# Performance work log

Hardware: AMD Instinct MI355X
Metric: run time of the kernel (lower is better)

## Reference

```python
import jax, jax.numpy as jnp
from jax import lax
import numpy as np

NUM_HEAD = 12
EPS = 1e-5            # torch LayerNorm default
NEG_INF = 1.0e12      # self.inf_value in the source
LEAKY_SLOPE = 0.01    # torch LeakyReLU default
MASK_FIRST = True     # maskedAtten=True applies only to block 0


def _layer_norm(x, s, b):
    m = jnp.mean(x, axis=-1, keepdims=True)
    v = jnp.var(x, axis=-1, keepdims=True)
    return (x - m) / jnp.sqrt(v + EPS) * s + b


def _forward(x, conv_w, conv_b, pos, ln0_s, ln0_b, Wq, bq, Wk, bk, Wv, bv,
             Wo, bo, ln1_s, ln1_b, W1, b1, W2, b2, proj_w, proj_b):
    B, C, H, W = x.shape
    E = conv_w.shape[0]
    P = conv_w.shape[-1]
    hd = E // NUM_HEAD

    # patch embed: Conv2d(C, E, P, stride=P)
    h = lax.conv_general_dilated(x, conv_w, (P, P), 'VALID',
                                 dimension_numbers=('NCHW', 'OIHW', 'NCHW'))
    h = h + conv_b[None, :, None, None]
    L = h.shape[2] * h.shape[3]
    h = h.reshape(B, E, L).transpose(0, 2, 1) + pos  # (B, L, E)

    causal = jnp.triu(jnp.ones((L, L), dtype=bool), 1)
    n_layers = Wq.shape[0]
    for i in range(n_layers):
        # --- attention block ---
        xn = _layer_norm(h, ln0_s[i], ln0_b[i])
        q = (xn @ Wq[i] + bq[i]).reshape(B, L, NUM_HEAD, hd).transpose(0, 2, 1, 3)
        k = (xn @ Wk[i] + bk[i]).reshape(B, L, NUM_HEAD, hd).transpose(0, 2, 1, 3)
        v = (xn @ Wv[i] + bv[i]).reshape(B, L, NUM_HEAD, hd).transpose(0, 2, 1, 3)
        scores = jnp.einsum('bhqd,bhkd->bhqk', q, k) * (hd ** -0.5)
        if i == 0 and MASK_FIRST:
            scores = jnp.where(causal, -NEG_INF, scores)
        a = jax.nn.softmax(scores, axis=-1)
        o = jnp.einsum('bhqk,bhkd->bhqd', a, v)  # (B, NH, L, hd)
        # faithful to torch source: reshape(bs, l, emb) WITHOUT permuting heads back
        o = o.reshape(B, L, E)
        o = o @ Wo[i] + bo[i]
        h = o + h  # residual onto pre-LN input
        # --- MLP block ---
        xr = _layer_norm(h, ln1_s[i], ln1_b[i])
        m = xr @ W1[i] + b1[i]
        m = jnp.where(m >= 0, m, LEAKY_SLOPE * m)
        m = m @ W2[i] + b2[i]
        h = m + xr  # residual onto post-LN (as in source)

    y = h @ proj_w + proj_b               # (B, L, C*P*P)
    y = y.transpose(0, 2, 1).reshape(B, C, H, W)
    return y


def setup_inputs() -> dict:
    key = jax.random.key(0)
    B, C, H, W = 8, 3, 384, 384
    P, E, NL = 16, 768, 8
    FF = 4 * E
    L = (H // P) * (W // P)  # 576
    CPP = C * P * P          # 768
    s = 0.02
    ks = jax.random.split(key, 24)
    f32 = jnp.float32
    inp = {
        'x': jax.random.normal(ks[0], (B, C, H, W), f32),
        'conv_w': jax.random.normal(ks[1], (E, C, P, P), f32) * s,
        'conv_b': jax.random.normal(ks[2], (E,), f32) * s,
        'pos': jax.random.normal(ks[3], (1, L, E), f32),
        'ln0_s': jnp.ones((NL, E), f32),
        'ln0_b': jnp.zeros((NL, E), f32),
        'Wq': jax.random.normal(ks[4], (NL, E, E), f32) * s,
        'bq': jax.random.normal(ks[5], (NL, E), f32) * s,
        'Wk': jax.random.normal(ks[6], (NL, E, E), f32) * s,
        'bk': jax.random.normal(ks[7], (NL, E), f32) * s,
        'Wv': jax.random.normal(ks[8], (NL, E, E), f32) * s,
        'bv': jax.random.normal(ks[9], (NL, E), f32) * s,
        'Wo': jax.random.normal(ks[10], (NL, E, E), f32) * s,
        'bo': jax.random.normal(ks[11], (NL, E), f32) * s,
        'ln1_s': jnp.ones((NL, E), f32),
        'ln1_b': jnp.zeros((NL, E), f32),
        'W1': jax.random.normal(ks[12], (NL, E, FF), f32) * s,
        'b1': jax.random.normal(ks[13], (NL, FF), f32) * s,
        'W2': jax.random.normal(ks[14], (NL, FF, E), f32) * s,
        'b2': jax.random.normal(ks[15], (NL, E), f32) * s,
        'proj_w': jax.random.normal(ks[16], (E, CPP), f32) * s,
        'proj_b': jax.random.normal(ks[17], (CPP,), f32) * s,
    }
    return inp


def reference(x, conv_w, conv_b, pos, ln0_s, ln0_b, Wq, bq, Wk, bk, Wv, bv,
              Wo, bo, ln1_s, ln1_b, W1, b1, W2, b2, proj_w, proj_b):
    return _forward(x, conv_w, conv_b, pos, ln0_s, ln0_b, Wq, bq, Wk, bk,
                    Wv, bv, Wo, bo, ln1_s, ln1_b, W1, b1, W2, b2,
                    proj_w, proj_b)
```

## Files before the change

### kernel.cpp

```cpp
#include <hip/hip_runtime.h>
#include <hip/hip_bf16.h>
#include <stdint.h>

#define NLAYERS 8
#define LSEQ 576
#define EMB 768
#define NHEAD 12
#define HDIM 64
#define FFDIM 3072
#define BLROWS 4608

typedef __attribute__((ext_vector_type(8))) short short8;
typedef __attribute__((ext_vector_type(4))) short short4v;
typedef __attribute__((ext_vector_type(4))) float floatx4;

__device__ __forceinline__ float b2f(short s) {
    union { float f; uint32_t u; } x; x.u = ((uint32_t)(uint16_t)s) << 16; return x.f;
}
__device__ __forceinline__ short f2b(float f) {
    union { float f; uint32_t u; } x; x.f = f;
    uint32_t r = x.u + 0x7fffu + ((x.u >> 16) & 1u);
    return (short)(r >> 16);
}

#define GLDS16(gp, lp) __builtin_amdgcn_global_load_lds( \
    (const __attribute__((address_space(1))) void*)(gp), \
    (__attribute__((address_space(3))) void*)(lp), 16, 0, 0)

__device__ __forceinline__ void xcd_remap(int& bx, int& by) {
    const int gx = gridDim.x;
    const int n  = gx * gridDim.y;
    const int orig = by * gx + bx;
    const int q = n >> 3, r = n & 7;
    const int xcd = orig & 7;
    const int wgid = (xcd < r ? xcd * (q + 1) : r * (q + 1) + (xcd - r) * q) + (orig >> 3);
    bx = wgid % gx;
    by = wgid / gx;
}

template<int DEPTH, int RES, bool ADD_POS, bool LEAKY, int OUTM, bool QKV, bool SPLITK>
__global__ __launch_bounds__(256)
void gemm_bt(const short* __restrict__ A, const short* __restrict__ Bt,
             const float* __restrict__ bias, const float* __restrict__ pos,
             const void* __restrict__ res, void* __restrict__ Cout,
             short* __restrict__ aux_kp, short* __restrict__ aux_vt,
             int N, int K)
{
    __shared__ short As[DEPTH * 64 * 64];
    __shared__ short Bs[DEPTH * 128 * 64];
    int bx = blockIdx.x, by = blockIdx.y;
    xcd_remap(bx, by);
    const int t    = threadIdx.x;
    const int lane = t & 63;
    const int w    = t >> 6;
    const int m0   = by * 64;
    const int n0   = bx * 128;
    const int wm   = (w >> 1) * 32;
    const int wn   = (w & 1) * 64;

    const int klen  = SPLITK ? (K >> 1) : K;
    const int kbase = SPLITK ? blockIdx.z * klen : 0;

    floatx4 acc[2][4];
#pragma unroll
    for (int i = 0; i < 2; ++i)
#pragma unroll
        for (int j = 0; j < 4; ++j)
            acc[i][j] = (floatx4){0.f, 0.f, 0.f, 0.f};

    const int srow = t >> 3;
    const int sch  = t & 7;
    const short* Ag = A  + (size_t)m0 * K + kbase;
    const short* Bg = Bt + (size_t)n0 * K + kbase;
    const int nt = klen >> 6;

#define STAGE(buf, k0)                                                              \
    {                                                                               \
        _Pragma("unroll")                                                           \
        for (int i = 0; i < 2; ++i) {                                               \
            int row = srow + i * 32;                                                \
            GLDS16(Ag + (size_t)row * K + (k0) + ((sch ^ (row & 7)) << 3),          \
                   &As[(buf) * 4096 + (size_t)(t + i * 256) * 8]);                  \
        }                                                                           \
        _Pragma("unroll")                                                           \
        for (int i = 0; i < 4; ++i) {                                               \
            int row = srow + i * 32;                                                \
            GLDS16(Bg + (size_t)row * K + (k0) + ((sch ^ (row & 7)) << 3),          \
                   &Bs[(buf) * 8192 + (size_t)(t + i * 256) * 8]);                  \
        }                                                                           \
    }

#define COMPUTE(buf)                                                                \
    {                                                                               \
        _Pragma("unroll")                                                           \
        for (int ks = 0; ks < 2; ++ks) {                                            \
            short8 af[2], bf[4];                                                    \
            _Pragma("unroll")                                                       \
            for (int i = 0; i < 2; ++i) {                                           \
                int row = wm + i * 16 + (lane & 15);                                \
                int ch  = (ks * 4 + (lane >> 4)) ^ (row & 7);                       \
                af[i] = *(const short8*)&As[(buf) * 4096 + row * 64 + ch * 8];      \
            }                                                                       \
            _Pragma("unroll")                                                       \
            for (int j = 0; j < 4; ++j) {                                           \
                int row = wn + j * 16 + (lane & 15);                                \
                int ch  = (ks * 4 + (lane >> 4)) ^ (row & 7);                       \
                bf[j] = *(const short8*)&Bs[(buf) * 8192 + row * 64 + ch * 8];      \
            }                                                                       \
            _Pragma("unroll")                                                       \
            for (int i = 0; i < 2; ++i)                                             \
                _Pragma("unroll")                                                   \
                for (int j = 0; j < 4; ++j)                                         \
                    acc[i][j] = __builtin_amdgcn_mfma_f32_16x16x32_bf16(            \
                        af[i], bf[j], acc[i][j], 0, 0, 0);                          \
        }                                                                           \
    }

    if constexpr (DEPTH == 2) {
        STAGE(0, 0);
        __syncthreads();
        int cur = 0;
        for (int k0 = 0; k0 < klen; k0 += 64) {
            if (k0 + 64 < klen) STAGE(cur ^ 1, k0 + 64);
            COMPUTE(cur);
            __syncthreads();
            cur ^= 1;
        }
    } else {
        STAGE(0, 0);
        STAGE(1, 64);
        asm volatile("s_waitcnt vmcnt(6)" ::: "memory");
        __builtin_amdgcn_sched_barrier(0);
        __builtin_amdgcn_s_barrier();
        int cur = 0, stg = 2;
        for (int tt = 0; tt < nt; ++tt) {
            if (tt + 2 < nt) STAGE(stg, (tt + 2) << 6);
            COMPUTE(cur);
            if (tt + 1 < nt) {
                if (tt + 2 < nt) { asm volatile("s_waitcnt vmcnt(6)" ::: "memory"); }
                else             { asm volatile("s_waitcnt vmcnt(0)" ::: "memory"); }
                __builtin_amdgcn_sched_barrier(0);
                __builtin_amdgcn_s_barrier();
                __builtin_amdgcn_sched_barrier(0);
            }
            cur = (cur + 1 == DEPTH) ? 0 : cur + 1;
            stg = (stg + 1 == DEPTH) ? 0 : stg + 1;
        }
    }
#undef STAGE
#undef COMPUTE

    const int colb = n0 + wn + (lane & 15);
    const int rowb = m0 + wm + ((lane >> 4) * 4);

    if constexpr (SPLITK) {
        float* P = blockIdx.z ? (float*)aux_kp : (float*)Cout;
#pragma unroll
        for (int i = 0; i < 2; ++i)
#pragma unroll
            for (int j = 0; j < 4; ++j)
#pragma unroll
                for (int r = 0; r < 4; ++r)
                    P[(size_t)(rowb + i * 16 + r) * N + colb + j * 16] = acc[i][j][r];
        return;
    }

#pragma unroll
    for (int i = 0; i < 2; ++i) {
#pragma unroll
        for (int j = 0; j < 4; ++j) {
            const int col = colb + j * 16;
            const float bv = bias[col];
#pragma unroll
            for (int r = 0; r < 4; ++r) {
                const int row = rowb + i * 16 + r;
                float v = acc[i][j][r] + bv;
                if constexpr (ADD_POS) v += pos[(size_t)(row % LSEQ) * N + col];
                if constexpr (RES == 1) v += ((const float*)res)[(size_t)row * N + col];
                if constexpr (RES == 2) v += b2f(((const short*)res)[(size_t)row * N + col]);
                if constexpr (LEAKY)   v = v >= 0.f ? v : 0.01f * v;
                if constexpr (QKV) {
                    const int b = row / LSEQ, l = row % LSEQ;
                    const short sv16 = f2b(v);
                    if (col < 768) {
                        ((short*)Cout)[(size_t)row * 768 + col] = sv16;
                    } else if (col < 1536) {
                        const int d = col - 768, hh = d >> 6, dd = d & 63;
                        const size_t bh = (size_t)b * 12 + hh;
                        aux_kp[(bh * LSEQ + l) * 64 + (dd & 7) + (((dd >> 3) ^ (l & 7)) << 3)] = sv16;
                    } else {
                        const int d = col - 1536, hh = d >> 6, dd = d & 63;
                        const size_t bh = (size_t)b * 12 + hh;
                        aux_vt[(bh * 64 + dd) * LSEQ + (l & ~63) + ((l & 63) ^ ((dd & 7) << 3))] = sv16;
                    }
                } else if constexpr (OUTM == 1) {
                    ((float*)Cout)[(size_t)row * N + col] = v;
                } else if constexpr (OUTM == 2) {
                    ((float*)Cout)[(size_t)row * N + col] = v;
                    aux_kp[(size_t)row * N + col] = f2b(v);
                } else {
                    ((short*)Cout)[(size_t)row * N + col] = f2b(v);
                }
            }
        }
    }
}

template<int RES, bool ADD_POS, int OUTM>
__global__ __launch_bounds__(256)
void combinek(const float* __restrict__ P0, const float* __restrict__ P1,
              const float* __restrict__ bias, const float* __restrict__ pos,
              const void* __restrict__ res, float* __restrict__ out,
              short* __restrict__ auxb)
{
    const size_t i4 = ((size_t)blockIdx.x * 256 + threadIdx.x) * 4;
    const int row = (int)(i4 / 768);
    const int col = (int)(i4 % 768);
    floatx4 a = *(const floatx4*)&P0[i4];
    floatx4 b = *(const floatx4*)&P1[i4];
    floatx4 bv = *(const floatx4*)&bias[col];
    floatx4 v;
#pragma unroll
    for (int j = 0; j < 4; ++j) v[j] = a[j] + b[j] + bv[j];
    if constexpr (ADD_POS) {
        floatx4 p = *(const floatx4*)&pos[(size_t)(row % LSEQ) * 768 + col];
#pragma unroll
        for (int j = 0; j < 4; ++j) v[j] += p[j];
    }
    if constexpr (RES == 1) {
        floatx4 rr = *(const floatx4*)&((const float*)res)[i4];
#pragma unroll
        for (int j = 0; j < 4; ++j) v[j] += rr[j];
    }
    if constexpr (RES == 2) {
        short4v rr = *(const short4v*)&((const short*)res)[i4];
#pragma unroll
        for (int j = 0; j < 4; ++j) v[j] += b2f(rr[j]);
    }
    *(floatx4*)&out[i4] = v;
    if constexpr (OUTM == 2) {
        short4v ob;
#pragma unroll
        for (int j = 0; j < 4; ++j) ob[j] = f2b(v[j]);
        *(short4v*)&auxb[i4] = ob;
    }
}

__global__ __launch_bounds__(256)
void ln_kernel(const float* __restrict__ h, const float* __restrict__ g,
               const float* __restrict__ bbias, short* __restrict__ outb)
{
    const int row = blockIdx.x;
    const float* x = h + (size_t)row * EMB;
    const int t = threadIdx.x;
    float v0 = x[t], v1 = x[t + 256], v2 = x[t + 512];
    float s  = v0 + v1 + v2;
    float ss = v0 * v0 + v1 * v1 + v2 * v2;
#pragma unroll
    for (int m = 1; m < 64; m <<= 1) {
        s  += __shfl_xor(s, m, 64);
        ss += __shfl_xor(ss, m, 64);
    }
    __shared__ float red[8];
    if ((t & 63) == 0) { red[t >> 6] = s; red[4 + (t >> 6)] = ss; }
    __syncthreads();
    float S  = red[0] + red[1] + red[2] + red[3];
    float SS = red[4] + red[5] + red[6] + red[7];
    float mean = S * (1.f / 768.f);
    float var  = SS * (1.f / 768.f) - mean * mean;
    float rstd = rsqrtf(var + 1e-5f);
    const size_t base = (size_t)row * EMB;
#pragma unroll
    for (int q = 0; q < 3; ++q) {
        int e = t + q * 256;
        float v = (q == 0 ? v0 : (q == 1 ? v1 : v2));
        float y = (v - mean) * rstd * g[e] + bbias[e];
        outb[base + e] = f2b(y);
    }
}

__global__ __launch_bounds__(256)
void attn_mfma(const short* __restrict__ qbuf, const short* __restrict__ kp,
               const short* __restrict__ vt, short* __restrict__ oout, int causal)
{
    const int qt = blockIdx.x, bh = blockIdx.y;
    const int b = bh / 12, h = bh % 12;
    const int t = threadIdx.x, lane = t & 63, w = t >> 6;

    __shared__ short Ks[64 * 64];
    __shared__ short Vs[64 * 64];
    __shared__ short Plds[4][16][72];

    const int nrow = lane & 15;
    const int kch  = (lane >> 4) * 8;
    const int swz  = (lane & 7) << 3;

    short8 aq[2];
    {
        const short* qrow = qbuf + ((size_t)(b * LSEQ) + qt * 64 + w * 16 + nrow) * 768 + h * 64 + kch;
        aq[0] = *(const short8*)qrow;
        aq[1] = *(const short8*)(qrow + 32);
    }

    float m[4], lsum[4];
    floatx4 oacc[4];
#pragma unroll
    for (int r = 0; r < 4; ++r) { m[r] = -3e38f; lsum[r] = 0.f; }
#pragma unroll
    for (int j = 0; j < 4; ++j) oacc[j] = (floatx4){0.f, 0.f, 0.f, 0.f};

    const int ktend = causal ? qt : 8;
    const short* ksrc = kp + ((size_t)bh * LSEQ) * 64;
    const short* vsrc = vt + ((size_t)bh * 64) * LSEQ;

    for (int kt = 0; kt <= ktend; ++kt) {
        __syncthreads();
        {
            const short* kt_src = ksrc + (size_t)(kt * 64) * 64;
            GLDS16(kt_src + (size_t)t * 8,          &Ks[(size_t)t * 8]);
            GLDS16(kt_src + (size_t)(t + 256) * 8,  &Ks[(size_t)(t + 256) * 8]);
            int f0 = t, f1 = t + 256;
            GLDS16(vsrc + (size_t)(f0 >> 3) * LSEQ + kt * 64 + (f0 & 7) * 8, &Vs[(size_t)f0 * 8]);
            GLDS16(vsrc + (size_t)(f1 >> 3) * LSEQ + kt * 64 + (f1 & 7) * 8, &Vs[(size_t)f1 * 8]);
        }
        __syncthreads();

        floatx4 sc[4];
#pragma unroll
        for (int j = 0; j < 4; ++j) sc[j] = (floatx4){0.f, 0.f, 0.f, 0.f};
#pragma unroll
        for (int s = 0; s < 2; ++s) {
#pragma unroll
            for (int j = 0; j < 4; ++j) {
                short8 bk = *(const short8*)&Ks[(16 * j + nrow) * 64 + ((kch + 32 * s) ^ swz)];
                sc[j] = __builtin_amdgcn_mfma_f32_16x16x32_bf16(aq[s], bk, sc[j], 0, 0, 0);
            }
        }
        float sv[4][4];
#pragma unroll
        for (int j = 0; j < 4; ++j)
#pragma unroll
            for (int r = 0; r < 4; ++r) {
                float v = sc[j][r] * 0.125f;
                if (causal && kt == qt) {
                    int key = kt * 64 + 16 * j + nrow;
                    int qr  = qt * 64 + w * 16 + (lane >> 4) * 4 + r;
                    if (key > qr) v = -1e12f;
                }
                sv[j][r] = v;
            }
#pragma unroll
        for (int r = 0; r < 4; ++r) {
            float tm = fmaxf(fmaxf(sv[0][r], sv[1][r]), fmaxf(sv[2][r], sv[3][r]));
            tm = fmaxf(tm, __shfl_xor(tm, 1, 64));
            tm = fmaxf(tm, __shfl_xor(tm, 2, 64));
            tm = fmaxf(tm, __shfl_xor(tm, 4, 64));
            tm = fmaxf(tm, __shfl_xor(tm, 8, 64));
            float nm = fmaxf(m[r], tm);
            float c  = __expf(m[r] - nm);
            m[r] = nm;
            float ps = 0.f;
#pragma unroll
            for (int j = 0; j < 4; ++j) {
                float p = __expf(sv[j][r] - nm);
                sv[j][r] = p;
                ps += p;
            }
            lsum[r] = lsum[r] * c + ps;
#pragma unroll
            for (int j = 0; j < 4; ++j) oacc[j][r] *= c;
        }
#pragma unroll
        for (int j = 0; j < 4; ++j)
#pragma unroll
            for (int r = 0; r < 4; ++r)
                Plds[w][(lane >> 4) * 4 + r][16 * j + nrow] = f2b(sv[j][r]);
        short8 ap[2];
#pragma unroll
        for (int s = 0; s < 2; ++s)
            ap[s] = *(const short8*)&Plds[w][nrow][kch + 32 * s];
#pragma unroll
        for (int s = 0; s < 2; ++s) {
#pragma unroll
            for (int j = 0; j < 4; ++j) {
                short8 bv = *(const short8*)&Vs[(16 * j + nrow) * 64 + ((kch + 32 * s) ^ swz)];
                oacc[j] = __builtin_amdgcn_mfma_f32_16x16x32_bf16(ap[s], bv, oacc[j], 0, 0, 0);
            }
        }
    }

    float inv[4];
#pragma unroll
    for (int r = 0; r < 4; ++r) {
        float L = lsum[r];
        L += __shfl_xor(L, 1, 64);
        L += __shfl_xor(L, 2, 64);
        L += __shfl_xor(L, 4, 64);
        L += __shfl_xor(L, 8, 64);
        inv[r] = 1.f / L;
    }
#pragma unroll
    for (int j = 0; j < 4; ++j)
#pragma unroll
        for (int r = 0; r < 4; ++r) {
            size_t lq = (size_t)qt * 64 + w * 16 + (lane >> 4) * 4 + r;
            oout[((size_t)bh * LSEQ + lq) * 64 + 16 * j + nrow] = f2b(oacc[j][r] * inv[r]);
        }
}

__global__ void transpose_f2b(const float* __restrict__ in, short* __restrict__ out,
                              int R, int C, long long ibs, long long obs)
{
    __shared__ float tile[32][33];
    const int b = blockIdx.z;
    const float* inb = in + (long long)b * ibs;
    short* outb = out + (long long)b * obs;
    const int r0 = blockIdx.y * 32, c0 = blockIdx.x * 32;
    const int tx = threadIdx.x, ty = threadIdx.y;
#pragma unroll
    for (int i = 0; i < 32; i += 8) tile[ty + i][tx] = inb[(size_t)(r0 + ty + i) * C + c0 + tx];
    __syncthreads();
#pragma unroll
    for (int i = 0; i < 32; i += 8) outb[(size_t)(c0 + ty + i) * R + r0 + tx] = f2b(tile[tx][ty + i]);
}

__global__ void transpose_f2f(const float* __restrict__ in, float* __restrict__ out,
                              int R, int C, long long ibs, long long obs)
{
    __shared__ float tile[32][33];
    const int b = blockIdx.z;
    const float* inb = in + (long long)b * ibs;
    float* outb = out + (long long)b * obs;
    const int r0 = blockIdx.y * 32, c0 = blockIdx.x * 32;
    const int tx = threadIdx.x, ty = threadIdx.y;
#pragma unroll
    for (int i = 0; i < 32; i += 8) tile[ty + i][tx] = inb[(size_t)(r0 + ty + i) * C + c0 + tx];
    __syncthreads();
#pragma unroll
    for (int i = 0; i < 32; i += 8) outb[(size_t)(c0 + ty + i) * R + r0 + tx] = tile[tx][ty + i];
}

__global__ void concat_qkv_bias(const float* __restrict__ bq, const float* __restrict__ bk,
                                const float* __restrict__ bv, float* __restrict__ out)
{
    int i = blockIdx.x * 256 + threadIdx.x;
    int layer = i / 2304, j = i % 2304;
    float v;
    if (j < 768)       v = bq[layer * 768 + j];
    else if (j < 1536) v = bk[layer * 768 + j - 768];
    else               v = bv[layer * 768 + j - 1536];
    out[i] = v;
}

__global__ void im2col_kernel(const float* __restrict__ x, short* __restrict__ xcol)
{
    const size_t idx = (size_t)blockIdx.x * 256 + threadIdx.x;
    const int k = (int)(idx % 768);
    const size_t m = idx / 768;
    const int c  = k >> 8;
    const int ky = (k >> 4) & 15;
    const int kx = k & 15;
    const int b  = (int)(m / 576);
    const int l  = (int)(m % 576);
    const int ph = l / 24, pw = l % 24;
    xcol[idx] = f2b(x[((size_t)(b * 3 + c) * 384 + ph * 16 + ky) * 384 + pw * 16 + kx]);
}

__global__ void cast_f32_b16(const float* __restrict__ in, short* __restrict__ out, int n)
{
    int i = blockIdx.x * 256 + threadIdx.x;
    if (i < n) out[i] = f2b(in[i]);
}

extern "C" void kernel_launch(void* const* d_in, const int* in_sizes, int n_in,
                              void* d_out, int out_size, void* d_ws, size_t ws_size,
                              hipStream_t stream)
{
    const float* x      = (const float*)d_in[0];
    const float* conv_w = (const float*)d_in[1];
    const float* conv_b = (const float*)d_in[2];
    const float* pos    = (const float*)d_in[3];
    const float* ln0_s  = (const float*)d_in[4];
    const float* ln0_b  = (const float*)d_in[5];
    const float* Wq     = (const float*)d_in[6];
    const float* bq     = (const float*)d_in[7];
    const float* Wk     = (const float*)d_in[8];
    const float* bk     = (const float*)d_in[9];
    const float* Wv     = (const float*)d_in[10];
    const float* bv     = (const float*)d_in[11];
    const float* Wo     = (const float*)d_in[12];
    const float* bo     = (const float*)d_in[13];
    const float* ln1_s  = (const float*)d_in[14];
    const float* ln1_b  = (const float*)d_in[15];
    const float* W1     = (const float*)d_in[16];
    const float* b1     = (const float*)d_in[17];
    const float* W2     = (const float*)d_in[18];
    const float* b2     = (const float*)d_in[19];
    const float* proj_w = (const float*)d_in[20];
    const float* proj_b = (const float*)d_in[21];

    char* ws = (char*)d_ws;
    short* qkvT  = (short*)(ws);
    short* woT   = (short*)(ws + 28311552);
    short* w1T   = (short*)(ws + 37748736);
    short* w2T   = (short*)(ws + 75497472);
    short* projT = (short*)(ws + 113246208);
    float* qkvb  = (float*)(ws + 114425856);
    short* tmpA  = (short*)(ws + 114499584);
    float* h     = (float*)(ws + 142811136);
    short* xn    = (short*)(ws + 156966912);
    short* xrb   = (short*)(ws + 164044800);
    short* qbuf  = (short*)(ws + 185278464);
    short* o     = (short*)(ws + 206512128);
    short* convB = (short*)(ws + 213590016);

    short* kp = tmpA;
    short* vt = tmpA + 3538944;
    float* P1 = (float*)qbuf;
    float* tmpAF = (float*)tmpA;

    dim3 tb(32, 8);
    transpose_f2b<<<dim3(24, 24, 8), tb, 0, stream>>>(Wq, qkvT,           768, 768, 589824, 1769472);
    transpose_f2b<<<dim3(24, 24, 8), tb, 0, stream>>>(Wk, qkvT + 589824,  768, 768, 589824, 1769472);
    transpose_f2b<<<dim3(24, 24, 8), tb, 0, stream>>>(Wv, qkvT + 1179648, 768, 768, 589824, 1769472);
    transpose_f2b<<<dim3(24, 24, 8), tb, 0, stream>>>(Wo, woT,            768, 768, 589824, 589824);
    transpose_f2b<<<dim3(96, 24, 8), tb, 0, stream>>>(W1, w1T,            768, 3072, 2359296, 2359296);
    transpose_f2b<<<dim3(24, 96, 8), tb, 0, stream>>>(W2, w2T,            3072, 768, 2359296, 2359296);
    transpose_f2b<<<dim3(24, 24, 1), tb, 0, stream>>>(proj_w, projT,      768, 768, 0, 0);
    cast_f32_b16<<<2304, 256, 0, stream>>>(conv_w, convB, 589824);
    concat_qkv_bias<<<72, 256, 0, stream>>>(bq, bk, bv, qkvb);

    im2col_kernel<<<13824, 256, 0, stream>>>(x, tmpA);
    gemm_bt<3, 0, false, false, 1, false, true><<<dim3(6, 72, 2), 256, 0, stream>>>(
        tmpA, convB, nullptr, nullptr, nullptr, h, (short*)P1, nullptr, 768, 768);
    combinek<0, true, 1><<<3456, 256, 0, stream>>>(h, P1, conv_b, pos, nullptr, h, nullptr);

    for (int i = 0; i < NLAYERS; ++i) {
        ln_kernel<<<4608, 256, 0, stream>>>(h, ln0_s + i * 768, ln0_b + i * 768, xn);
        gemm_bt<2, 0, false, false, 0, true, false><<<dim3(18, 72), 256, 0, stream>>>(
            xn, qkvT + (size_t)i * 1769472, qkvb + i * 2304, nullptr, nullptr, qbuf, kp, vt, 2304, 768);
        attn_mfma<<<dim3(9, 96), 256, 0, stream>>>(qbuf, kp, vt, o, i == 0 ? 1 : 0);
        gemm_bt<3, 0, false, false, 1, false, true><<<dim3(6, 72, 2), 256, 0, stream>>>(
            o, woT + (size_t)i * 589824, nullptr, nullptr, nullptr, tmpAF, (short*)P1, nullptr, 768, 768);
        combinek<1, false, 1><<<3456, 256, 0, stream>>>(tmpAF, P1, bo + i * 768, nullptr, h, h, nullptr);
        ln_kernel<<<4608, 256, 0, stream>>>(h, ln1_s + i * 768, ln1_b + i * 768, xrb);
        gemm_bt<2, 0, false, true, 0, false, false><<<dim3(24, 72), 256, 0, stream>>>(
            xrb, w1T + (size_t)i * 2359296, b1 + i * 3072, nullptr, nullptr, tmpA, nullptr, nullptr, 3072, 768);
        gemm_bt<3, 0, false, false, 1, false, true><<<dim3(6, 72, 2), 256, 0, stream>>>(
            tmpA, w2T + (size_t)i * 2359296, nullptr, nullptr, nullptr, h, (short*)P1, nullptr, 768, 3072);
        if (i < NLAYERS - 1) {
            combinek<2, false, 1><<<3456, 256, 0, stream>>>(h, P1, b2 + i * 768, nullptr, xrb, h, nullptr);
        } else {
            combinek<2, false, 2><<<3456, 256, 0, stream>>>(h, P1, b2 + i * 768, nullptr, xrb, h, xn);
        }
    }

    short* hb = xn;
    float* yf = tmpAF;
    gemm_bt<3, 0, false, false, 1, false, true><<<dim3(6, 72, 2), 256, 0, stream>>>(
        hb, projT, nullptr, nullptr, nullptr, h, (short*)P1, nullptr, 768, 768);
    combinek<0, false, 1><<<3456, 256, 0, stream>>>(h, P1, proj_b, nullptr, nullptr, yf, nullptr);
    transpose_f2f<<<dim3(24, 18, 8), tb, 0, stream>>>(yf, (float*)d_out, 576, 768, 442368, 442368);
}
```

Baseline: 1.780 ms.

## Drop split-K for K=768 GEMMs and add 128x128 split-K kernel for W2

The conv-embed, Wo and projection GEMMs (K=768) no longer split K in two. They write their epilogue (bias, pos, residual) directly, which removes the separate combine kernel and its partial-sum round trip through memory. The K=3072 W2 GEMM moves to a new dedicated split-K kernel with 128x128 tiles and 4x4 MFMA accumulators per wave, raising data reuse per block. The trade-off is fewer blocks for the 768-wide GEMMs (432 instead of 864) and higher register use in the new kernel.

```diff
diff --git a/kernel.cpp b/kernel.cpp
--- a/kernel.cpp
+++ b/kernel.cpp
@@ -38,7 +38,7 @@
     by = wgid / gx;
 }
 
-template<int DEPTH, int RES, bool ADD_POS, bool LEAKY, int OUTM, bool QKV, bool SPLITK>
+template<int DEPTH, int RES, bool ADD_POS, bool LEAKY, int OUTM, bool QKV>
 __global__ __launch_bounds__(256)
 void gemm_bt(const short* __restrict__ A, const short* __restrict__ Bt,
              const float* __restrict__ bias, const float* __restrict__ pos,
@@ -58,9 +58,6 @@
     const int wm   = (w >> 1) * 32;
     const int wn   = (w & 1) * 64;
 
-    const int klen  = SPLITK ? (K >> 1) : K;
-    const int kbase = SPLITK ? blockIdx.z * klen : 0;
-
     floatx4 acc[2][4];
 #pragma unroll
     for (int i = 0; i < 2; ++i)
@@ -70,9 +67,9 @@
 
     const int srow = t >> 3;
     const int sch  = t & 7;
-    const short* Ag = A  + (size_t)m0 * K + kbase;
-    const short* Bg = Bt + (size_t)n0 * K + kbase;
-    const int nt = klen >> 6;
+    const short* Ag = A  + (size_t)m0 * K;
+    const short* Bg = Bt + (size_t)n0 * K;
+    const int nt = K >> 6;
 
 #define STAGE(buf, k0)                                                              \
     {                                                                               \
@@ -120,8 +117,8 @@
         STAGE(0, 0);
         __syncthreads();
         int cur = 0;
-        for (int k0 = 0; k0 < klen; k0 += 64) {
-            if (k0 + 64 < klen) STAGE(cur ^ 1, k0 + 64);
+        for (int k0 = 0; k0 < K; k0 += 64) {
+            if (k0 + 64 < K) STAGE(cur ^ 1, k0 + 64);
             COMPUTE(cur);
             __syncthreads();
             cur ^= 1;
@@ -152,19 +149,6 @@
 
     const int colb = n0 + wn + (lane & 15);
     const int rowb = m0 + wm + ((lane >> 4) * 4);
-
-    if constexpr (SPLITK) {
-        float* P = blockIdx.z ? (float*)aux_kp : (float*)Cout;
-#pragma unroll
-        for (int i = 0; i < 2; ++i)
-#pragma unroll
-            for (int j = 0; j < 4; ++j)
-#pragma unroll
-                for (int r = 0; r < 4; ++r)
-                    P[(size_t)(rowb + i * 16 + r) * N + colb + j * 16] = acc[i][j][r];
-        return;
-    }
-
 #pragma unroll
     for (int i = 0; i < 2; ++i) {
 #pragma unroll
@@ -206,6 +190,95 @@
     }
 }
 
+__global__ __launch_bounds__(256)
+void gemm_sk2(const short* __restrict__ A, const short* __restrict__ Bt,
+              float* __restrict__ P0, float* __restrict__ P1, int N, int K)
+{
+    __shared__ short As[2 * 128 * 64];
+    __shared__ short Bs[2 * 128 * 64];
+    int bx = blockIdx.x, by = blockIdx.y;
+    xcd_remap(bx, by);
+    const int t    = threadIdx.x;
+    const int lane = t & 63;
+    const int w    = t >> 6;
+    const int m0   = by * 128;
+    const int n0   = bx * 128;
+    const int wm   = (w >> 1) * 64;
+    const int wn   = (w & 1) * 64;
+    const int klen  = K >> 1;
+    const int kbase = blockIdx.z * klen;
+
+    floatx4 acc[4][4];
+#pragma unroll
+    for (int i = 0; i < 4; ++i)
+#pragma unroll
+        for (int j = 0; j < 4; ++j)
+            acc[i][j] = (floatx4){0.f, 0.f, 0.f, 0.f};
+
+    const int srow = t >> 3;
+    const int sch  = t & 7;
+    const short* Ag = A  + (size_t)m0 * K + kbase;
+    const short* Bg = Bt + (size_t)n0 * K + kbase;
+
+#define STAGE(buf, k0)                                                              \
+    {                                                                               \
+        _Pragma("unroll")                                                           \
+        for (int i = 0; i < 4; ++i) {                                               \
+            int row = srow + i * 32;                                                \
+            GLDS16(Ag + (size_t)row * K + (k0) + ((sch ^ (row & 7)) << 3),          \
+                   &As[(buf) * 8192 + (size_t)(t + i * 256) * 8]);                  \
+        }                                                                           \
+        _Pragma("unroll")                                                           \
+        for (int i = 0; i < 4; ++i) {                                               \
+            int row = srow + i * 32;                                                \
+            GLDS16(Bg + (size_t)row * K + (k0) + ((sch ^ (row & 7)) << 3),          \
+                   &Bs[(buf) * 8192 + (size_t)(t + i * 256) * 8]);                  \
+        }                                                                           \
+    }
+
+    STAGE(0, 0);
+    __syncthreads();
+    int cur = 0;
+    for (int k0 = 0; k0 < klen; k0 += 64) {
+        if (k0 + 64 < klen) STAGE(cur ^ 1, k0 + 64);
+#pragma unroll
+        for (int ks = 0; ks < 2; ++ks) {
+            short8 af[4], bf[4];
+#pragma unroll
+            for (int i = 0; i < 4; ++i) {
+                int row = wm + i * 16 + (lane & 15);
+                int ch  = (ks * 4 + (lane >> 4)) ^ (row & 7);
+                af[i] = *(const short8*)&As[cur * 8192 + row * 64 + ch * 8];
+            }
+#pragma unroll
+            for (int j = 0; j < 4; ++j) {
+                int row = wn + j * 16 + (lane & 15);
+                int ch  = (ks * 4 + (lane >> 4)) ^ (row & 7);
+                bf[j] = *(const short8*)&Bs[cur * 8192 + row * 64 + ch * 8];
+            }
+#pragma unroll
+            for (int i = 0; i < 4; ++i)
+#pragma unroll
+                for (int j = 0; j < 4; ++j)
+                    acc[i][j] = __builtin_amdgcn_mfma_f32_16x16x32_bf16(af[i], bf[j], acc[i][j], 0, 0, 0);
+        }
+        __syncthreads();
+        cur ^= 1;
+    }
+#undef STAGE
+
+    float* P = blockIdx.z ? P1 : P0;
+    const int colb = n0 + wn + (lane & 15);
+    const int rowb = m0 + wm + ((lane >> 4) * 4);
+#pragma unroll
+    for (int i = 0; i < 4; ++i)
+#pragma unroll
+        for (int j = 0; j < 4; ++j)
+#pragma unroll
+            for (int r = 0; r < 4; ++r)
+                P[(size_t)(rowb + i * 16 + r) * N + colb + j * 16] = acc[i][j][r];
+}
+
 template<int RES, bool ADD_POS, int OUTM>
 __global__ __launch_bounds__(256)
 void combinek(const float* __restrict__ P0, const float* __restrict__ P1,
@@ -517,7 +590,6 @@
     short* kp = tmpA;
     short* vt = tmpA + 3538944;
     float* P1 = (float*)qbuf;
-    float* tmpAF = (float*)tmpA;
 
     dim3 tb(32, 8);
     transpose_f2b<<<dim3(24, 24, 8), tb, 0, stream>>>(Wq, qkvT,           768, 768, 589824, 1769472);
@@ -531,23 +603,21 @@
     concat_qkv_bias<<<72, 256, 0, stream>>>(bq, bk, bv, qkvb);
 
     im2col_kernel<<<13824, 256, 0, stream>>>(x, tmpA);
-    gemm_bt<3, 0, false, false, 1, false, true><<<dim3(6, 72, 2), 256, 0, stream>>>(
-        tmpA, convB, nullptr, nullptr, nullptr, h, (short*)P1, nullptr, 768, 768);
-    combinek<0, true, 1><<<3456, 256, 0, stream>>>(h, P1, conv_b, pos, nullptr, h, nullptr);
+    gemm_bt<3, 0, true, false, 1, false><<<dim3(6, 72), 256, 0, stream>>>(
+        tmpA, convB, conv_b, pos, nullptr, h, nullptr, nullptr, 768, 768);
 
     for (int i = 0; i < NLAYERS; ++i) {
         ln_kernel<<<4608, 256, 0, stream>>>(h, ln0_s + i * 768, ln0_b + i * 768, xn);
-        gemm_bt<2, 0, false, false, 0, true, false><<<dim3(18, 72), 256, 0, stream>>>(
+        gemm_bt<2, 0, false, false, 0, true><<<dim3(18, 72), 256, 0, stream>>>(
             xn, qkvT + (size_t)i * 1769472, qkvb + i * 2304, nullptr, nullptr, qbuf, kp, vt, 2304, 768);
         attn_mfma<<<dim3(9, 96), 256, 0, stream>>>(qbuf, kp, vt, o, i == 0 ? 1 : 0);
-        gemm_bt<3, 0, false, false, 1, false, true><<<dim3(6, 72, 2), 256, 0, stream>>>(
-            o, woT + (size_t)i * 589824, nullptr, nullptr, nullptr, tmpAF, (short*)P1, nullptr, 768, 768);
-        combinek<1, false, 1><<<3456, 256, 0, stream>>>(tmpAF, P1, bo + i * 768, nullptr, h, h, nullptr);
+        gemm_bt<3, 1, false, false, 1, false><<<dim3(6, 72), 256, 0, stream>>>(
+            o, woT + (size_t)i * 589824, bo + i * 768, nullptr, h, h, nullptr, nullptr, 768, 768);
         ln_kernel<<<4608, 256, 0, stream>>>(h, ln1_s + i * 768, ln1_b + i * 768, xrb);
-        gemm_bt<2, 0, false, true, 0, false, false><<<dim3(24, 72), 256, 0, stream>>>(
+        gemm_bt<2, 0, false, true, 0, false><<<dim3(24, 72), 256, 0, stream>>>(
             xrb, w1T + (size_t)i * 2359296, b1 + i * 3072, nullptr, nullptr, tmpA, nullptr, nullptr, 3072, 768);
-        gemm_bt<3, 0, false, false, 1, false, true><<<dim3(6, 72, 2), 256, 0, stream>>>(
-            tmpA, w2T + (size_t)i * 2359296, nullptr, nullptr, nullptr, h, (short*)P1, nullptr, 768, 3072);
+        gemm_sk2<<<dim3(6, 36, 2), 256, 0, stream>>>(
+            tmpA, w2T + (size_t)i * 2359296, h, P1, 768, 3072);
         if (i < NLAYERS - 1) {
             combinek<2, false, 1><<<3456, 256, 0, stream>>>(h, P1, b2 + i * 768, nullptr, xrb, h, nullptr);
         } else {
@@ -556,9 +626,8 @@
     }
 
     short* hb = xn;
-    float* yf = tmpAF;
-    gemm_bt<3, 0, false, false, 1, false, true><<<dim3(6, 72, 2), 256, 0, stream>>>(
-        hb, projT, nullptr, nullptr, nullptr, h, (short*)P1, nullptr, 768, 768);
-    combinek<0, false, 1><<<3456, 256, 0, stream>>>(h, P1, proj_b, nullptr, nullptr, yf, nullptr);
+    float* yf = (float*)tmpA;
+    gemm_bt<3, 0, false, false, 1, false><<<dim3(6, 72), 256, 0, stream>>>(
+        hb, projT, proj_b, nullptr, nullptr, yf, nullptr, nullptr, 768, 768);
     transpose_f2f<<<dim3(24, 18, 8), tb, 0, stream>>>(yf, (float*)d_out, 576, 768, 442368, 442368);
 }
```

Measured after the change: 1.593 ms. 1.12x faster.
